# Kernel tuning notes

Hardware: AMD Instinct MI355X
Metric: run time of the kernel (lower is better)

## Reference

```python
import jax, jax.numpy as jnp
import numpy as np


def setup_inputs() -> dict:
    key = jax.random.key(0)
    k1, k2 = jax.random.split(key)
    B, N, D = 32, 8192, 64
    x = jax.random.normal(k1, (B, N, D), dtype=jnp.float32)
    y = jax.random.normal(k2, (B, D, N), dtype=jnp.float32)
    return {"x": x, "y": y}


def reference(x, y):
    # Original: full cdist [B,N,N], mean over batch, take diagonal.
    # Only matched pairs (i,i) survive, so compute them directly —
    # mathematically identical output and gradients.
    y_t = jnp.transpose(y, (0, 2, 1))          # [B, N, D]
    diff = x - y_t                             # [B, N, D]
    pair_dist = jnp.sqrt(jnp.sum(diff * diff, axis=-1))  # [B, N]
    dist_diag = jnp.mean(pair_dist, axis=0)    # [N] == diag(mean_b cdist)
    dist_diag = dist_diag.at[1:3].multiply(1.5)
    loss = jnp.mean(dist_diag)
    return loss
```

## Files before the change

### kernel.cpp

```cpp
#include <hip/hip_runtime.h>


constexpr int B  = 32;
constexpr int N  = 8192;
constexpr int D  = 64;
constexpr int TN = 64;
constexpr int NBLK = (N / TN) * B;

#define GLD_LDS(gp, lp, sz)                                                              \
    __builtin_amdgcn_global_load_lds(                                                    \
        (const __attribute__((address_space(1))) void*)(gp),                             \
        (__attribute__((address_space(3))) void*)(lp), (sz), 0, 0)

__global__ __launch_bounds__(256) void euclid_loss_kernel(
    const float* __restrict__ x,
    const float* __restrict__ y,
    float* __restrict__ ws)
{
    __shared__ float x_s[TN * D];
    __shared__ float y_s[D * TN];

    const int tid  = threadIdx.x;
    const int wave = tid >> 6;
    const int lane = tid & 63;
    const int n0   = blockIdx.x * TN;
    const int b    = blockIdx.y;

    const float* xg = x + ((size_t)b * N + n0) * D;
    const float* yg = y + (size_t)b * D * N + n0;

#pragma unroll
    for (int j = 0; j < 4; ++j) {
        const int c = wave * 4 + j;
        GLD_LDS(xg + c * 256 + lane * 4, x_s + c * 256, 16);
    }
#pragma unroll
    for (int j = 0; j < 16; ++j) {
        const int d = wave * 16 + j;
        GLD_LDS(yg + (size_t)d * N + lane, y_s + d * TN, 4);
    }

    __syncthreads();

    float acc = 0.0f;
#pragma unroll
    for (int s = 0; s < 16; ++s) {
        const int d  = wave * 16 + ((lane + s) & 15);
        const float df = x_s[lane * D + d] - y_s[d * TN + lane];
        acc += df * df;
    }

    __syncthreads();
    x_s[wave * TN + lane] = acc;
    __syncthreads();

    if (tid < TN) {
        const float s = x_s[tid] + x_s[TN + tid] + x_s[2 * TN + tid] + x_s[3 * TN + tid];
        const int   n = n0 + tid;
        const float w = (n == 1 || n == 2) ? 1.5f : 1.0f;
        float v = w * __builtin_sqrtf(s);
#pragma unroll
        for (int off = 32; off > 0; off >>= 1) v += __shfl_down(v, off, 64);
        if (tid == 0)
            ws[blockIdx.y * gridDim.x + blockIdx.x] = v;
    }
}

__global__ __launch_bounds__(256) void reduce_kernel(
    const float* __restrict__ ws,
    float* __restrict__ out)
{
    const int tid = threadIdx.x;
    float v = 0.0f;
#pragma unroll
    for (int j = 0; j < NBLK / (256 * 4); ++j) {
        const float4 p = *reinterpret_cast<const float4*>(ws + j * 1024 + tid * 4);
        v += p.x + p.y + p.z + p.w;
    }
#pragma unroll
    for (int off = 32; off > 0; off >>= 1) v += __shfl_down(v, off, 64);

    __shared__ float wsum[4];
    if ((tid & 63) == 0) wsum[tid >> 6] = v;
    __syncthreads();
    if (tid == 0)
        out[0] = (wsum[0] + wsum[1] + wsum[2] + wsum[3]) * (1.0f / (float)(B * N));
}

extern "C" void kernel_launch(void* const* d_in, const int* in_sizes, int n_in,
                              void* d_out, int out_size, void* d_ws, size_t ws_size,
                              hipStream_t stream) {
    const float* x = (const float*)d_in[0];
    const float* y = (const float*)d_in[1];
    float* out = (float*)d_out;
    float* ws  = (float*)d_ws;

    dim3 grid(N / TN, B);
    euclid_loss_kernel<<<grid, 256, 0, stream>>>(x, y, ws);
    reduce_kernel<<<1, 256, 0, stream>>>(ws, out);
}
```

Before: 141.8 us.

## Replace LDS staging with direct float4 register loads and larger N tiles

```diff
diff --git a/kernel.cpp b/kernel.cpp
--- a/kernel.cpp
+++ b/kernel.cpp
@@ -4,64 +4,83 @@
 constexpr int B  = 32;
 constexpr int N  = 8192;
 constexpr int D  = 64;
-constexpr int TN = 64;
+constexpr int TN = 256;
 constexpr int NBLK = (N / TN) * B;
-
-#define GLD_LDS(gp, lp, sz)                                                              \
-    __builtin_amdgcn_global_load_lds(                                                    \
-        (const __attribute__((address_space(1))) void*)(gp),                             \
-        (__attribute__((address_space(3))) void*)(lp), (sz), 0, 0)
 
 __global__ __launch_bounds__(256) void euclid_loss_kernel(
     const float* __restrict__ x,
     const float* __restrict__ y,
     float* __restrict__ ws)
 {
-    __shared__ float x_s[TN * D];
-    __shared__ float y_s[D * TN];
+    const int tid = threadIdx.x;
+    const int ds  = tid >> 6;
+    const int g   = tid & 63;
+    const int n0  = blockIdx.x * TN;
+    const int b   = blockIdx.y;
+    const int ng  = n0 + 4 * g;
+    const int d0  = ds * 16;
 
-    const int tid  = threadIdx.x;
-    const int wave = tid >> 6;
-    const int lane = tid & 63;
-    const int n0   = blockIdx.x * TN;
-    const int b    = blockIdx.y;
+    const float* xp = x + ((size_t)b * N + ng) * D + d0;
+    const float* yp = y + ((size_t)b * D + d0) * N + ng;
 
-    const float* xg = x + ((size_t)b * N + n0) * D;
-    const float* yg = y + (size_t)b * D * N + n0;
+    float acc0 = 0.f, acc1 = 0.f, acc2 = 0.f, acc3 = 0.f;
 
 #pragma unroll
     for (int j = 0; j < 4; ++j) {
-        const int c = wave * 4 + j;
-        GLD_LDS(xg + c * 256 + lane * 4, x_s + c * 256, 16);
-    }
-#pragma unroll
-    for (int j = 0; j < 16; ++j) {
-        const int d = wave * 16 + j;
-        GLD_LDS(yg + (size_t)d * N + lane, y_s + d * TN, 4);
+        const int dd = 4 * j;
+        const float4 y0 = *reinterpret_cast<const float4*>(yp + (size_t)(dd + 0) * N);
+        const float4 y1 = *reinterpret_cast<const float4*>(yp + (size_t)(dd + 1) * N);
+        const float4 y2 = *reinterpret_cast<const float4*>(yp + (size_t)(dd + 2) * N);
+        const float4 y3 = *reinterpret_cast<const float4*>(yp + (size_t)(dd + 3) * N);
+        const float4 x0 = *reinterpret_cast<const float4*>(xp + 0 * D + dd);
+        const float4 x1 = *reinterpret_cast<const float4*>(xp + 1 * D + dd);
+        const float4 x2 = *reinterpret_cast<const float4*>(xp + 2 * D + dd);
+        const float4 x3 = *reinterpret_cast<const float4*>(xp + 3 * D + dd);
+
+        float d;
+        d = x0.x - y0.x; acc0 += d * d;  d = x0.y - y1.x; acc0 += d * d;
+        d = x0.z - y2.x; acc0 += d * d;  d = x0.w - y3.x; acc0 += d * d;
+        d = x1.x - y0.y; acc1 += d * d;  d = x1.y - y1.y; acc1 += d * d;
+        d = x1.z - y2.y; acc1 += d * d;  d = x1.w - y3.y; acc1 += d * d;
+        d = x2.x - y0.z; acc2 += d * d;  d = x2.y - y1.z; acc2 += d * d;
+        d = x2.z - y2.z; acc2 += d * d;  d = x2.w - y3.z; acc2 += d * d;
+        d = x3.x - y0.w; acc3 += d * d;  d = x3.y - y1.w; acc3 += d * d;
+        d = x3.z - y2.w; acc3 += d * d;  d = x3.w - y3.w; acc3 += d * d;
     }
 
+    __shared__ float4 part[4][64];
+    part[ds][g] = make_float4(acc0, acc1, acc2, acc3);
     __syncthreads();
 
-    float acc = 0.0f;
-#pragma unroll
-    for (int s = 0; s < 16; ++s) {
-        const int d  = wave * 16 + ((lane + s) & 15);
-        const float df = x_s[lane * D + d] - y_s[d * TN + lane];
-        acc += df * df;
-    }
-
-    __syncthreads();
-    x_s[wave * TN + lane] = acc;
-    __syncthreads();
-
-    if (tid < TN) {
-        const float s = x_s[tid] + x_s[TN + tid] + x_s[2 * TN + tid] + x_s[3 * TN + tid];
-        const int   n = n0 + tid;
-        const float w = (n == 1 || n == 2) ? 1.5f : 1.0f;
-        float v = w * __builtin_sqrtf(s);
+    if (ds == 0) {
+        const float4 p0 = part[0][g];
+        const float4 p1 = part[1][g];
+        const float4 p2 = part[2][g];
+        const float4 p3 = part[3][g];
+        float v = 0.f;
+        {
+            const float s = p0.x + p1.x + p2.x + p3.x;
+            const int   n = ng + 0;
+            v += ((n == 1 || n == 2) ? 1.5f : 1.0f) * __builtin_sqrtf(s);
+        }
+        {
+            const float s = p0.y + p1.y + p2.y + p3.y;
+            const int   n = ng + 1;
+            v += ((n == 1 || n == 2) ? 1.5f : 1.0f) * __builtin_sqrtf(s);
+        }
+        {
+            const float s = p0.z + p1.z + p2.z + p3.z;
+            const int   n = ng + 2;
+            v += ((n == 1 || n == 2) ? 1.5f : 1.0f) * __builtin_sqrtf(s);
+        }
+        {
+            const float s = p0.w + p1.w + p2.w + p3.w;
+            const int   n = ng + 3;
+            v += ((n == 1 || n == 2) ? 1.5f : 1.0f) * __builtin_sqrtf(s);
+        }
 #pragma unroll
         for (int off = 32; off > 0; off >>= 1) v += __shfl_down(v, off, 64);
-        if (tid == 0)
+        if (g == 0)
             ws[blockIdx.y * gridDim.x + blockIdx.x] = v;
     }
 }
@@ -71,12 +90,8 @@
     float* __restrict__ out)
 {
     const int tid = threadIdx.x;
-    float v = 0.0f;
-#pragma unroll
-    for (int j = 0; j < NBLK / (256 * 4); ++j) {
-        const float4 p = *reinterpret_cast<const float4*>(ws + j * 1024 + tid * 4);
-        v += p.x + p.y + p.z + p.w;
-    }
+    const float4 p = *reinterpret_cast<const float4*>(ws + tid * 4);
+    float v = p.x + p.y + p.z + p.w;
 #pragma unroll
     for (int off = 32; off > 0; off >>= 1) v += __shfl_down(v, off, 64);
 
```

New measurement: 151.4 us. +6.8%, slower.

## Load x and y directly into registers with float4 tiles, drop LDS staging

Applied to the files above, without the earlier changes.

```diff
diff --git a/kernel.cpp b/kernel.cpp
--- a/kernel.cpp
+++ b/kernel.cpp
@@ -4,66 +4,85 @@
 constexpr int B  = 32;
 constexpr int N  = 8192;
 constexpr int D  = 64;
-constexpr int TN = 64;
+constexpr int TN = 128;
 constexpr int NBLK = (N / TN) * B;
-
-#define GLD_LDS(gp, lp, sz)                                                              \
-    __builtin_amdgcn_global_load_lds(                                                    \
-        (const __attribute__((address_space(1))) void*)(gp),                             \
-        (__attribute__((address_space(3))) void*)(lp), (sz), 0, 0)
 
 __global__ __launch_bounds__(256) void euclid_loss_kernel(
     const float* __restrict__ x,
     const float* __restrict__ y,
     float* __restrict__ ws)
 {
-    __shared__ float x_s[TN * D];
-    __shared__ float y_s[D * TN];
+    const int tid = threadIdx.x;
+    const int w   = tid >> 6;
+    const int g   = tid & 63;
+    const int c   = g & 15;
+    const int dw  = g >> 4;
+    const int nh  = w >> 1;
+    const int dh  = w & 1;
+    const int n0  = blockIdx.x * TN;
+    const int b   = blockIdx.y;
+    const int nb  = n0 + nh * 64 + 4 * c;
+    const int d0  = dh * 32 + dw * 8;
 
-    const int tid  = threadIdx.x;
-    const int wave = tid >> 6;
-    const int lane = tid & 63;
-    const int n0   = blockIdx.x * TN;
-    const int b    = blockIdx.y;
+    const float* xp = x + ((size_t)b * N + nb) * D + d0;
+    const float* yp = y + ((size_t)b * D + d0) * N + nb;
 
-    const float* xg = x + ((size_t)b * N + n0) * D;
-    const float* yg = y + (size_t)b * D * N + n0;
+    float4 xr[4][2];
+#pragma unroll
+    for (int r = 0; r < 4; ++r) {
+        xr[r][0] = *reinterpret_cast<const float4*>(xp + r * D + 0);
+        xr[r][1] = *reinterpret_cast<const float4*>(xp + r * D + 4);
+    }
+    float4 yv[8];
+#pragma unroll
+    for (int jd = 0; jd < 8; ++jd)
+        yv[jd] = *reinterpret_cast<const float4*>(yp + (size_t)jd * N);
 
+    float acc[4] = {0.f, 0.f, 0.f, 0.f};
+#define ACC_R(r, CMP)                                          \
+    { float t;                                                 \
+      t = xr[r][0].x - yv[0].CMP; acc[r] += t * t;             \
+      t = xr[r][0].y - yv[1].CMP; acc[r] += t * t;             \
+      t = xr[r][0].z - yv[2].CMP; acc[r] += t * t;             \
+      t = xr[r][0].w - yv[3].CMP; acc[r] += t * t;             \
+      t = xr[r][1].x - yv[4].CMP; acc[r] += t * t;             \
+      t = xr[r][1].y - yv[5].CMP; acc[r] += t * t;             \
+      t = xr[r][1].z - yv[6].CMP; acc[r] += t * t;             \
+      t = xr[r][1].w - yv[7].CMP; acc[r] += t * t; }
+    ACC_R(0, x)
+    ACC_R(1, y)
+    ACC_R(2, z)
+    ACC_R(3, w)
+#undef ACC_R
+
+    __shared__ float partF[2][4][128];
+    *reinterpret_cast<float4*>(&partF[dh][dw][nh * 64 + 4 * c]) =
+        make_float4(acc[0], acc[1], acc[2], acc[3]);
+    __syncthreads();
+
+    float v = 0.f;
+    if (tid < TN) {
+        const int nh2 = tid >> 6;
+        const int m   = tid & 63;
+        float s = 0.f;
 #pragma unroll
-    for (int j = 0; j < 4; ++j) {
-        const int c = wave * 4 + j;
-        GLD_LDS(xg + c * 256 + lane * 4, x_s + c * 256, 16);
+        for (int dh2 = 0; dh2 < 2; ++dh2)
+#pragma unroll
+            for (int dw2 = 0; dw2 < 4; ++dw2)
+                s += partF[dh2][dw2][nh2 * 64 + m];
+        const int n = n0 + tid;
+        const float wt = (n == 1 || n == 2) ? 1.5f : 1.0f;
+        v = wt * __builtin_sqrtf(s);
     }
 #pragma unroll
-    for (int j = 0; j < 16; ++j) {
-        const int d = wave * 16 + j;
-        GLD_LDS(yg + (size_t)d * N + lane, y_s + d * TN, 4);
-    }
+    for (int off = 32; off > 0; off >>= 1) v += __shfl_down(v, off, 64);
 
+    __shared__ float wsum[4];
+    if ((tid & 63) == 0) wsum[tid >> 6] = v;
     __syncthreads();
-
-    float acc = 0.0f;
-#pragma unroll
-    for (int s = 0; s < 16; ++s) {
-        const int d  = wave * 16 + ((lane + s) & 15);
-        const float df = x_s[lane * D + d] - y_s[d * TN + lane];
-        acc += df * df;
-    }
-
-    __syncthreads();
-    x_s[wave * TN + lane] = acc;
-    __syncthreads();
-
-    if (tid < TN) {
-        const float s = x_s[tid] + x_s[TN + tid] + x_s[2 * TN + tid] + x_s[3 * TN + tid];
-        const int   n = n0 + tid;
-        const float w = (n == 1 || n == 2) ? 1.5f : 1.0f;
-        float v = w * __builtin_sqrtf(s);
-#pragma unroll
-        for (int off = 32; off > 0; off >>= 1) v += __shfl_down(v, off, 64);
-        if (tid == 0)
-            ws[blockIdx.y * gridDim.x + blockIdx.x] = v;
-    }
+    if (tid == 0)
+        ws[blockIdx.y * gridDim.x + blockIdx.x] =
+            wsum[0] + wsum[1] + wsum[2] + wsum[3];
 }
 
 __global__ __launch_bounds__(256) void reduce_kernel(
@@ -71,7 +90,7 @@
     float* __restrict__ out)
 {
     const int tid = threadIdx.x;
-    float v = 0.0f;
+    float v = 0.f;
 #pragma unroll
     for (int j = 0; j < NBLK / (256 * 4); ++j) {
         const float4 p = *reinterpret_cast<const float4*>(ws + j * 1024 + tid * 4);
```

Result: no change. 141.7 us (-0.1%).
